# Optimization experiments

Measured on AMD Instinct MI355X. Metric: run time of the kernel, lower is better.

Reference implementation:

```python
import jax, jax.numpy as jnp
import numpy as np

D_MODEL = 1024
N_HEADS = 16
D_K = D_MODEL // N_HEADS


def _xavier(key, shape):
    fan_in, fan_out = shape[1], shape[0]
    a = np.sqrt(6.0 / (fan_in + fan_out))
    return jax.random.uniform(key, shape, jnp.float32, -a, a)


def setup_inputs() -> dict:
    key = jax.random.key(0)
    kx, kq, kk, kv, ko = jax.random.split(key, 5)
    x = jax.random.normal(kx, (2, 2048, D_MODEL), jnp.float32)
    # nn.Linear weights are [out, in]; y = x @ W.T
    Wq = _xavier(kq, (D_MODEL, D_MODEL))
    Wk = _xavier(kk, (D_MODEL, D_MODEL))
    Wv = _xavier(kv, (D_MODEL, D_MODEL))
    Wo = _xavier(ko, (D_MODEL, D_MODEL))
    bo = jnp.zeros((D_MODEL,), jnp.float32)
    return {"x": x, "Wq": Wq, "Wk": Wk, "Wv": Wv, "Wo": Wo, "bo": bo}


def reference(x, Wq, Wk, Wv, Wo, bo):
    B, S, D = x.shape
    def split_heads(t):
        # [B,S,D] -> [B,H,S,d_k]
        return t.reshape(B, S, N_HEADS, D_K).transpose(0, 2, 1, 3)
    Q = split_heads(x @ Wq.T)
    K = split_heads(x @ Wk.T)
    V = split_heads(x @ Wv.T)
    scale = 1.0 / jnp.sqrt(jnp.asarray(D_K, x.dtype))
    scores = jnp.einsum('bhqd,bhkd->bhqk', Q, K) * scale  # [B,H,S,S]
    attn = jax.nn.softmax(scores, axis=-1)
    out = jnp.einsum('bhqk,bhkd->bhqd', attn, V)  # [B,H,S,d_k]
    out = out.transpose(0, 2, 1, 3).reshape(B, S, D)  # merge heads
    return out @ Wo.T + bo
```

## Files before the change

### kernel.cpp

```cpp
#include <hip/hip_runtime.h>


typedef __attribute__((ext_vector_type(8))) short bf16x8;
typedef __attribute__((ext_vector_type(4))) short bf16x4;
typedef __attribute__((ext_vector_type(4))) float f32x4;
typedef __attribute__((ext_vector_type(2))) unsigned int u32x2;
typedef __attribute__((ext_vector_type(4))) unsigned int u32x4;

#define GK 1024
#define SEQ 2048
#define NHEAD 16
#define DKD 64
#define PADW 72

#define MFMA32(a, b, c) __builtin_amdgcn_mfma_f32_16x16x32_bf16((a), (b), (c), 0, 0, 0)

#if __has_builtin(__builtin_amdgcn_exp2f)
#define EXP2(x) __builtin_amdgcn_exp2f(x)
#else
#define EXP2(x) exp2f(x)
#endif

#define QSCALE 0.18033688011f

static __device__ __forceinline__ unsigned short f2bf(float f) {
    unsigned int u = __float_as_uint(f);
    u += 0x7fffu + ((u >> 16) & 1u);
    return (unsigned short)(u >> 16);
}

static __device__ __forceinline__ unsigned int pack_bf2(float a, float b) {
    unsigned int ua = __float_as_uint(a) + 0x8000u;
    unsigned int ub = __float_as_uint(b) + 0x8000u;
    return __builtin_amdgcn_perm(ub, ua, 0x07060302u);
}

__global__ __launch_bounds__(256) void cast_all(const float* __restrict__ x,
                                                const float* __restrict__ wq,
                                                const float* __restrict__ wk,
                                                const float* __restrict__ wv,
                                                const float* __restrict__ wo,
                                                unsigned short* __restrict__ Xb,
                                                unsigned short* __restrict__ Wqkv,
                                                unsigned short* __restrict__ Wob) {
    const int bid = blockIdx.x;
    const float* src; unsigned short* dst; int off;
    if (bid < 4096)      { src = x;  dst = Xb;             off = bid; }
    else if (bid < 5120) { src = wq; dst = Wqkv;           off = bid - 4096; }
    else if (bid < 6144) { src = wk; dst = Wqkv + 1048576; off = bid - 5120; }
    else if (bid < 7168) { src = wv; dst = Wqkv + 2097152; off = bid - 6144; }
    else                 { src = wo; dst = Wob;            off = bid - 7168; }
    const int i = off * 1024 + threadIdx.x * 4;
    float4 v = *(const float4*)(src + i);
    u32x2 p; p.x = pack_bf2(v.x, v.y); p.y = pack_bf2(v.z, v.w);
    *(u32x2*)(dst + i) = p;
}

template <int MODE, int BN>
__global__ __launch_bounds__(256) void gemm_bt(const unsigned short* __restrict__ A,
                                               const unsigned short* __restrict__ Bw,
                                               unsigned short* __restrict__ outb,
                                               float* __restrict__ outf,
                                               const float* __restrict__ bias) {
    constexpr int NJ = BN / 32;
    constexpr int LOOP_BYTES = 128 * 64 * 2 + BN * 64 * 2;
    constexpr int EPI_BYTES  = 4 * 64 * PADW * 2;
    constexpr int SMEM_BYTES = (MODE == 0)
        ? (LOOP_BYTES > EPI_BYTES ? LOOP_BYTES : EPI_BYTES)
        : LOOP_BYTES;
    __shared__ __align__(16) unsigned char SMEM[SMEM_BYTES];
    unsigned short* As = (unsigned short*)SMEM;
    unsigned short* Bs = As + 128 * 64;

    const int t    = threadIdx.x;
    const int lane = t & 63;
    const int w    = t >> 6;
    const int wm   = (w >> 1) * 64;
    const int wn   = (w & 1) * (BN / 2);
    const int bm0  = blockIdx.x * 128;
    const int bn0  = blockIdx.y * BN;
    const int lm   = lane & 15;
    const int lq   = lane >> 4;
    const int swzb = lm & 7;

    const unsigned short* Ab = A + (size_t)bm0 * GK;
    const unsigned short* Bb = Bw + (size_t)bn0 * GK;

    f32x4 acc[4][NJ];
    const f32x4 Z4 = {0.f, 0.f, 0.f, 0.f};
#pragma unroll
    for (int i = 0; i < 4; i++)
#pragma unroll
        for (int j = 0; j < NJ; j++) acc[i][j] = Z4;

    const int q_uni = (t & ~63);

    for (int k0 = 0; k0 < GK; k0 += 64) {
        __syncthreads();
#pragma unroll
        for (int i = 0; i < 4; ++i) {
            int q  = i * 256 + t;
            int r  = q >> 3;
            int gc = (q & 7) ^ (r & 7);
            int q0 = i * 256 + q_uni;
            __builtin_amdgcn_global_load_lds(
                (const __attribute__((address_space(1))) void*)(Ab + (size_t)r * GK + k0 + gc * 8),
                (__attribute__((address_space(3))) void*)(As + (size_t)q0 * 8),
                16, 0, 0);
        }
#pragma unroll
        for (int i = 0; i < BN / 32; ++i) {
            int q  = i * 256 + t;
            int r  = q >> 3;
            int gc = (q & 7) ^ (r & 7);
            int q0 = i * 256 + q_uni;
            __builtin_amdgcn_global_load_lds(
                (const __attribute__((address_space(1))) void*)(Bb + (size_t)r * GK + k0 + gc * 8),
                (__attribute__((address_space(3))) void*)(Bs + (size_t)q0 * 8),
                16, 0, 0);
        }
        __syncthreads();

#pragma unroll
        for (int kk = 0; kk < 2; ++kk) {
            const int swz = ((kk * 4 + lq) ^ swzb) * 8;
            bf16x8 af[4], bf[NJ];
#pragma unroll
            for (int i = 0; i < 4; i++)
                af[i] = *(const bf16x8*)(As + (wm + i * 16 + lm) * 64 + swz);
#pragma unroll
            for (int j = 0; j < NJ; j++)
                bf[j] = *(const bf16x8*)(Bs + (wn + j * 16 + lm) * 64 + swz);
#pragma unroll
            for (int i = 0; i < 4; i++)
#pragma unroll
                for (int j = 0; j < NJ; j++)
                    acc[i][j] = MFMA32(af[i], bf[j], acc[i][j]);
        }
    }

    if (MODE == 0) {
        __syncthreads();
        unsigned short* E  = (unsigned short*)SMEM;
        unsigned short* Ew = E + w * (64 * PADW);
        const int nbase = bn0 + wn;
        const int which = nbase >> 10;
        const int hh    = (nbase & 1023) >> 6;
        if (which != 2) {
            const float sc = (which == 0) ? QSCALE : 1.0f;
#pragma unroll
            for (int i = 0; i < 4; i++)
#pragma unroll
                for (int j = 0; j < 4; j++)
#pragma unroll
                    for (int r = 0; r < 4; r++)
                        Ew[(i * 16 + lq * 4 + r) * PADW + j * 16 + lm] =
                            f2bf(acc[i][j][r] * sc);
            unsigned short* dst = outb + (size_t)which * 4194304;
#pragma unroll
            for (int rep = 0; rep < 8; ++rep) {
                const int mm = rep * 8 + (lane >> 3);
                const int d0 = (lane & 7) * 8;
                uint4 v = *(const uint4*)(Ew + mm * PADW + d0);
                const int m_g = bm0 + wm + mm;
                const int b = m_g >> 11, s = m_g & 2047;
                *(uint4*)(dst + (((size_t)(b * NHEAD + hh)) * SEQ + s) * DKD + d0) = v;
            }
        } else {
#pragma unroll
            for (int i = 0; i < 4; i++)
#pragma unroll
                for (int j = 0; j < 4; j++) {
                    u32x2 pk;
                    pk.x = pack_bf2(acc[i][j][0], acc[i][j][1]);
                    pk.y = pack_bf2(acc[i][j][2], acc[i][j][3]);
                    *(u32x2*)(Ew + (j * 16 + lm) * PADW + i * 16 + lq * 4) = pk;
                }
            unsigned short* dst = outb + (size_t)2 * 4194304;
#pragma unroll
            for (int rep = 0; rep < 8; ++rep) {
                const int nn = rep * 8 + (lane >> 3);
                const int mc = (lane & 7) * 8;
                uint4 v = *(const uint4*)(Ew + nn * PADW + mc);
                const int m_g = bm0 + wm + mc;
                const int b = m_g >> 11, s0 = m_g & 2047;
                *(uint4*)(dst + (((size_t)(b * NHEAD + hh)) * DKD + nn) * SEQ + s0) = v;
            }
        }
    } else {
#pragma unroll
        for (int i = 0; i < 4; i++) {
            const int mbase = bm0 + wm + i * 16 + lq * 4;
#pragma unroll
            for (int j = 0; j < NJ; j++) {
                const int n = bn0 + wn + j * 16 + lm;
#pragma unroll
                for (int r = 0; r < 4; r++)
                    outf[(size_t)(mbase + r) * 1024 + n] = acc[i][j][r] + bias[n];
            }
        }
    }
}

__global__ __launch_bounds__(256, 4) void attn_kernel(const unsigned short* __restrict__ Qg,
                                                      const unsigned short* __restrict__ Kg,
                                                      const unsigned short* __restrict__ Vtg,
                                                      unsigned short* __restrict__ Og) {
    __shared__ __align__(16) unsigned short KV[2][2][64 * PADW];

    const int id  = blockIdx.x;
    const int xcd = id & 7;
    const int j8  = id >> 3;
    const int bh  = xcd * 4 + (j8 & 3);
    const int qb  = j8 >> 2;
    const unsigned short* Qp  = Qg  + ((size_t)bh * SEQ + qb * 64) * DKD;
    const unsigned short* Kp  = Kg  + (size_t)bh * SEQ * DKD;
    const unsigned short* Vtp = Vtg + (size_t)bh * DKD * SEQ;

    const int t    = threadIdx.x;
    const int lane = t & 63;
    const int w    = t >> 6;
    const int qg   = w >> 1;
    const int kg   = w & 1;
    const int lm   = lane & 15;
    const int kq   = lane >> 4;

    const f32x4 Z4 = {0.f, 0.f, 0.f, 0.f};

    bf16x8 aq[2][2];
#pragma unroll
    for (int c = 0; c < 2; ++c)
#pragma unroll
        for (int kk = 0; kk < 2; ++kk)
            aq[c][kk] = *(const bf16x8*)(Qp + (size_t)(qg * 32 + c * 16 + lm) * DKD + kk * 32 + kq * 8);

    f32x4 o[2][4];
    float ls[2];
#pragma unroll
    for (int c = 0; c < 2; ++c) {
        ls[c] = 0.f;
#pragma unroll
        for (int dj = 0; dj < 4; ++dj) o[c][dj] = Z4;
    }

    const int sr = t >> 2, sc = (t & 3) * 16;
    uint4 kreg0, kreg1, vreg0, vreg1;
    {
        const unsigned short* kp = Kp + (size_t)sr * DKD + sc;
        const unsigned short* vp = Vtp + (size_t)sr * SEQ + sc;
        uint4 a0 = *(const uint4*)(kp), a1 = *(const uint4*)(kp + 8);
        uint4 b0 = *(const uint4*)(vp), b1 = *(const uint4*)(vp + 8);
        uint4* dk = (uint4*)(&KV[0][0][sr * PADW + sc]); dk[0] = a0; dk[1] = a1;
        uint4* dv = (uint4*)(&KV[0][1][sr * PADW + sc]); dv[0] = b0; dv[1] = b1;
    }
    {
        const unsigned short* kp = Kp + (size_t)(64 + sr) * DKD + sc;
        kreg0 = *(const uint4*)(kp); kreg1 = *(const uint4*)(kp + 8);
        const unsigned short* vp = Vtp + (size_t)sr * SEQ + 64 + sc;
        vreg0 = *(const uint4*)(vp); vreg1 = *(const uint4*)(vp + 8);
    }

    for (int kt = 0; kt < 32; ++kt) {
        asm volatile("s_waitcnt lgkmcnt(0)\n\ts_barrier" ::: "memory");
        const unsigned short* Kc = &KV[kt & 1][0][0];
        const unsigned short* Vc = &KV[kt & 1][1][0];

        bf16x8 ak[2][2];
#pragma unroll
        for (int kc = 0; kc < 2; ++kc)
#pragma unroll
            for (int kk = 0; kk < 2; ++kk)
                ak[kc][kk] = *(const bf16x8*)(Kc + (kg * 32 + kc * 16 + lm) * PADW + kk * 32 + kq * 8);

        if (kt + 1 < 32) {
            uint4* dk = (uint4*)(&KV[(kt + 1) & 1][0][sr * PADW + sc]);
            dk[0] = kreg0; dk[1] = kreg1;
            uint4* dv = (uint4*)(&KV[(kt + 1) & 1][1][sr * PADW + sc]);
            dv[0] = vreg0; dv[1] = vreg1;
        }
        if (kt + 2 < 32) {
            const unsigned short* kp = Kp + (size_t)((kt + 2) * 64 + sr) * DKD + sc;
            kreg0 = *(const uint4*)(kp); kreg1 = *(const uint4*)(kp + 8);
            const unsigned short* vp = Vtp + (size_t)sr * SEQ + (kt + 2) * 64 + sc;
            vreg0 = *(const uint4*)(vp); vreg1 = *(const uint4*)(vp + 8);
        }

        f32x4 s[2][2];
        __builtin_amdgcn_s_setprio(1);
#pragma unroll
        for (int kc = 0; kc < 2; ++kc)
#pragma unroll
            for (int c = 0; c < 2; ++c) {
                s[kc][c] = MFMA32(ak[kc][0], aq[c][0], Z4);
                s[kc][c] = MFMA32(ak[kc][1], aq[c][1], s[kc][c]);
            }
        __builtin_amdgcn_s_setprio(0);

        bf16x8 bv[4];
#pragma unroll
        for (int dj = 0; dj < 4; ++dj) {
            const unsigned short* vr = Vc + (dj * 16 + lm) * PADW + kg * 32;
            u32x2 lo = __builtin_bit_cast(u32x2, *(const bf16x4*)(vr + kq * 4));
            u32x2 hi = __builtin_bit_cast(u32x2, *(const bf16x4*)(vr + 16 + kq * 4));
            u32x4 uu; uu.x = lo.x; uu.y = lo.y; uu.z = hi.x; uu.w = hi.y;
            bv[dj] = __builtin_bit_cast(bf16x8, uu);
        }

#pragma unroll
        for (int c = 0; c < 2; ++c) {
#pragma unroll
            for (int kc = 0; kc < 2; ++kc)
#pragma unroll
                for (int r = 0; r < 4; ++r) s[kc][c][r] = EXP2(s[kc][c][r]);
            ls[c] += ((s[0][c][0] + s[0][c][1]) + (s[0][c][2] + s[0][c][3]))
                   + ((s[1][c][0] + s[1][c][1]) + (s[1][c][2] + s[1][c][3]));
        }

        bf16x8 pa[2];
#pragma unroll
        for (int c = 0; c < 2; ++c) {
            u32x4 uu;
            uu.x = pack_bf2(s[0][c][0], s[0][c][1]);
            uu.y = pack_bf2(s[0][c][2], s[0][c][3]);
            uu.z = pack_bf2(s[1][c][0], s[1][c][1]);
            uu.w = pack_bf2(s[1][c][2], s[1][c][3]);
            pa[c] = __builtin_bit_cast(bf16x8, uu);
        }

        __builtin_amdgcn_s_setprio(1);
#pragma unroll
        for (int dj = 0; dj < 4; ++dj)
#pragma unroll
            for (int c = 0; c < 2; ++c)
                o[c][dj] = MFMA32(pa[c], bv[dj], o[c][dj]);
        __builtin_amdgcn_s_setprio(0);
    }

    __syncthreads();
    float* Lf = (float*)(&KV[0][0][0]);

#pragma unroll
    for (int c = 0; c < 2; ++c) {
        float v = ls[c];
        v += __shfl_xor(v, 16);
        v += __shfl_xor(v, 32);
        if (kq == 0) Lf[w * 32 + c * 16 + lm] = v;
    }
    __syncthreads();

    const int rq = t >> 2;
    const int dq = (t & 3) * 8;
    const int qgr = rq >> 5, qlr = rq & 31;
    float li = Lf[qgr * 64 + qlr] + Lf[qgr * 64 + 32 + qlr];
#if __has_builtin(__builtin_amdgcn_rcpf)
    li = __builtin_amdgcn_rcpf(li);
#else
    li = 1.0f / li;
#endif
    __syncthreads();

    const int b = bh >> 4, h = bh & 15;
#pragma unroll
    for (int p = 0; p < 2; ++p) {
#pragma unroll
        for (int c = 0; c < 2; ++c)
#pragma unroll
            for (int djh = 0; djh < 2; ++djh) {
                const int dj = 2 * p + djh;
#pragma unroll
                for (int r = 0; r < 4; ++r)
                    Lf[(w * 32 + c * 16 + kq * 4 + r) * 36 + djh * 16 + lm] = o[c][dj][r];
            }
        __syncthreads();
        f32x4 a0 = *(const f32x4*)(Lf + (qgr * 64 + qlr) * 36 + dq)
                 + *(const f32x4*)(Lf + (qgr * 64 + 32 + qlr) * 36 + dq);
        f32x4 a1 = *(const f32x4*)(Lf + (qgr * 64 + qlr) * 36 + dq + 4)
                 + *(const f32x4*)(Lf + (qgr * 64 + 32 + qlr) * 36 + dq + 4);
        uint4 outv;
        outv.x = pack_bf2(a0[0] * li, a0[1] * li);
        outv.y = pack_bf2(a0[2] * li, a0[3] * li);
        outv.z = pack_bf2(a1[0] * li, a1[1] * li);
        outv.w = pack_bf2(a1[2] * li, a1[3] * li);
        *(uint4*)(Og + (((size_t)(b * SEQ + qb * 64 + rq)) * NHEAD + h) * DKD + p * 32 + dq) = outv;
        __syncthreads();
    }
}

extern "C" void kernel_launch(void* const* d_in, const int* in_sizes, int n_in,
                              void* d_out, int out_size, void* d_ws, size_t ws_size,
                              hipStream_t stream) {
    const float* x  = (const float*)d_in[0];
    const float* Wq = (const float*)d_in[1];
    const float* Wk = (const float*)d_in[2];
    const float* Wv = (const float*)d_in[3];
    const float* Wo = (const float*)d_in[4];
    const float* bo = (const float*)d_in[5];
    float* out = (float*)d_out;

    unsigned short* ws = (unsigned short*)d_ws;
    unsigned short* Xb   = ws;
    unsigned short* Wqkv = ws + 4194304;
    unsigned short* Wob  = ws + 7340032;
    unsigned short* QKV  = ws + 8388608;
    unsigned short* Ob   = ws + 20971520;

    cast_all<<<8192, 256, 0, stream>>>(x, Wq, Wk, Wv, Wo, Xb, Wqkv, Wob);
    gemm_bt<0, 128><<<dim3(32, 24), 256, 0, stream>>>(Xb, Wqkv, QKV, nullptr, nullptr);
    attn_kernel<<<1024, 256, 0, stream>>>(QKV, QKV + 4194304, QKV + 8388608, Ob);
    gemm_bt<1, 64><<<dim3(32, 16), 256, 0, stream>>>(Ob, Wob, nullptr, out, bo);
}
```

Before: 187.5 us.

## Process 128 query rows per attention block to reuse K/V tiles

Each attention block now handles two 64-row query halves against the same K/V tiles staged in shared memory. This halves the grid to 512 blocks and halves the total K/V global and LDS staging traffic per query row. The cost is doubled accumulator and Q register state, with the launch-bounds occupancy hint lowered from 4 to 2. Fewer blocks are also available to fill the GPU.

```diff
diff --git a/kernel.cpp b/kernel.cpp
--- a/kernel.cpp
+++ b/kernel.cpp
@@ -202,7 +202,7 @@
     }
 }
 
-__global__ __launch_bounds__(256, 4) void attn_kernel(const unsigned short* __restrict__ Qg,
+__global__ __launch_bounds__(256, 2) void attn_kernel(const unsigned short* __restrict__ Qg,
                                                       const unsigned short* __restrict__ Kg,
                                                       const unsigned short* __restrict__ Vtg,
                                                       unsigned short* __restrict__ Og) {
@@ -213,7 +213,7 @@
     const int j8  = id >> 3;
     const int bh  = xcd * 4 + (j8 & 3);
     const int qb  = j8 >> 2;
-    const unsigned short* Qp  = Qg  + ((size_t)bh * SEQ + qb * 64) * DKD;
+    const unsigned short* Qp  = Qg  + ((size_t)bh * SEQ + qb * 128) * DKD;
     const unsigned short* Kp  = Kg  + (size_t)bh * SEQ * DKD;
     const unsigned short* Vtp = Vtg + (size_t)bh * DKD * SEQ;
 
@@ -227,21 +227,25 @@
 
     const f32x4 Z4 = {0.f, 0.f, 0.f, 0.f};
 
-    bf16x8 aq[2][2];
-#pragma unroll
-    for (int c = 0; c < 2; ++c)
-#pragma unroll
-        for (int kk = 0; kk < 2; ++kk)
-            aq[c][kk] = *(const bf16x8*)(Qp + (size_t)(qg * 32 + c * 16 + lm) * DKD + kk * 32 + kq * 8);
-
-    f32x4 o[2][4];
-    float ls[2];
-#pragma unroll
-    for (int c = 0; c < 2; ++c) {
-        ls[c] = 0.f;
-#pragma unroll
-        for (int dj = 0; dj < 4; ++dj) o[c][dj] = Z4;
-    }
+    bf16x8 aq[2][2][2];
+#pragma unroll
+    for (int h2 = 0; h2 < 2; ++h2)
+#pragma unroll
+        for (int c = 0; c < 2; ++c)
+#pragma unroll
+            for (int kk = 0; kk < 2; ++kk)
+                aq[h2][c][kk] = *(const bf16x8*)(Qp + (size_t)(h2 * 64 + qg * 32 + c * 16 + lm) * DKD + kk * 32 + kq * 8);
+
+    f32x4 o[2][2][4];
+    float ls[2][2];
+#pragma unroll
+    for (int h2 = 0; h2 < 2; ++h2)
+#pragma unroll
+        for (int c = 0; c < 2; ++c) {
+            ls[h2][c] = 0.f;
+#pragma unroll
+            for (int dj = 0; dj < 4; ++dj) o[h2][c][dj] = Z4;
+        }
 
     const int sr = t >> 2, sc = (t & 3) * 16;
     uint4 kreg0, kreg1, vreg0, vreg1;
@@ -285,17 +289,6 @@
             vreg0 = *(const uint4*)(vp); vreg1 = *(const uint4*)(vp + 8);
         }
 
-        f32x4 s[2][2];
-        __builtin_amdgcn_s_setprio(1);
-#pragma unroll
-        for (int kc = 0; kc < 2; ++kc)
-#pragma unroll
-            for (int c = 0; c < 2; ++c) {
-                s[kc][c] = MFMA32(ak[kc][0], aq[c][0], Z4);
-                s[kc][c] = MFMA32(ak[kc][1], aq[c][1], s[kc][c]);
-            }
-        __builtin_amdgcn_s_setprio(0);
-
         bf16x8 bv[4];
 #pragma unroll
         for (int dj = 0; dj < 4; ++dj) {
@@ -307,81 +300,106 @@
         }
 
 #pragma unroll
-        for (int c = 0; c < 2; ++c) {
+        for (int h2 = 0; h2 < 2; ++h2) {
+            f32x4 s[2][2];
+            __builtin_amdgcn_s_setprio(1);
 #pragma unroll
             for (int kc = 0; kc < 2; ++kc)
 #pragma unroll
-                for (int r = 0; r < 4; ++r) s[kc][c][r] = EXP2(s[kc][c][r]);
-            ls[c] += ((s[0][c][0] + s[0][c][1]) + (s[0][c][2] + s[0][c][3]))
-                   + ((s[1][c][0] + s[1][c][1]) + (s[1][c][2] + s[1][c][3]));
-        }
-
-        bf16x8 pa[2];
-#pragma unroll
-        for (int c = 0; c < 2; ++c) {
-            u32x4 uu;
-            uu.x = pack_bf2(s[0][c][0], s[0][c][1]);
-            uu.y = pack_bf2(s[0][c][2], s[0][c][3]);
-            uu.z = pack_bf2(s[1][c][0], s[1][c][1]);
-            uu.w = pack_bf2(s[1][c][2], s[1][c][3]);
-            pa[c] = __builtin_bit_cast(bf16x8, uu);
-        }
-
-        __builtin_amdgcn_s_setprio(1);
-#pragma unroll
-        for (int dj = 0; dj < 4; ++dj)
-#pragma unroll
-            for (int c = 0; c < 2; ++c)
-                o[c][dj] = MFMA32(pa[c], bv[dj], o[c][dj]);
-        __builtin_amdgcn_s_setprio(0);
+                for (int c = 0; c < 2; ++c) {
+                    s[kc][c] = MFMA32(ak[kc][0], aq[h2][c][0], Z4);
+                    s[kc][c] = MFMA32(ak[kc][1], aq[h2][c][1], s[kc][c]);
+                }
+            __builtin_amdgcn_s_setprio(0);
+
+#pragma unroll
+            for (int c = 0; c < 2; ++c) {
+#pragma unroll
+                for (int kc = 0; kc < 2; ++kc)
+#pragma unroll
+                    for (int r = 0; r < 4; ++r) s[kc][c][r] = EXP2(s[kc][c][r]);
+                ls[h2][c] += ((s[0][c][0] + s[0][c][1]) + (s[0][c][2] + s[0][c][3]))
+                           + ((s[1][c][0] + s[1][c][1]) + (s[1][c][2] + s[1][c][3]));
+            }
+
+            bf16x8 pa[2];
+#pragma unroll
+            for (int c = 0; c < 2; ++c) {
+                u32x4 uu;
+                uu.x = pack_bf2(s[0][c][0], s[0][c][1]);
+                uu.y = pack_bf2(s[0][c][2], s[0][c][3]);
+                uu.z = pack_bf2(s[1][c][0], s[1][c][1]);
+                uu.w = pack_bf2(s[1][c][2], s[1][c][3]);
+                pa[c] = __builtin_bit_cast(bf16x8, uu);
+            }
+
+            __builtin_amdgcn_s_setprio(1);
+#pragma unroll
+            for (int dj = 0; dj < 4; ++dj)
+#pragma unroll
+                for (int c = 0; c < 2; ++c)
+                    o[h2][c][dj] = MFMA32(pa[c], bv[dj], o[h2][c][dj]);
+            __builtin_amdgcn_s_setprio(0);
+        }
     }
 
     __syncthreads();
     float* Lf = (float*)(&KV[0][0][0]);
 
 #pragma unroll
-    for (int c = 0; c < 2; ++c) {
-        float v = ls[c];
-        v += __shfl_xor(v, 16);
-        v += __shfl_xor(v, 32);
-        if (kq == 0) Lf[w * 32 + c * 16 + lm] = v;
-    }
+    for (int h2 = 0; h2 < 2; ++h2)
+#pragma unroll
+        for (int c = 0; c < 2; ++c) {
+            float v = ls[h2][c];
+            v += __shfl_xor(v, 16);
+            v += __shfl_xor(v, 32);
+            if (kq == 0) Lf[(h2 * 4 + w) * 32 + c * 16 + lm] = v;
+        }
     __syncthreads();
 
     const int rq = t >> 2;
     const int dq = (t & 3) * 8;
     const int qgr = rq >> 5, qlr = rq & 31;
-    float li = Lf[qgr * 64 + qlr] + Lf[qgr * 64 + 32 + qlr];
+    float li[2];
+#pragma unroll
+    for (int h2 = 0; h2 < 2; ++h2) {
+        float l = Lf[(h2 * 4 + qgr * 2) * 32 + qlr] + Lf[(h2 * 4 + qgr * 2 + 1) * 32 + qlr];
 #if __has_builtin(__builtin_amdgcn_rcpf)
-    li = __builtin_amdgcn_rcpf(li);
+        li[h2] = __builtin_amdgcn_rcpf(l);
 #else
-    li = 1.0f / li;
+        li[h2] = 1.0f / l;
 #endif
+    }
     __syncthreads();
 
     const int b = bh >> 4, h = bh & 15;
 #pragma unroll
     for (int p = 0; p < 2; ++p) {
 #pragma unroll
-        for (int c = 0; c < 2; ++c)
-#pragma unroll
-            for (int djh = 0; djh < 2; ++djh) {
-                const int dj = 2 * p + djh;
-#pragma unroll
-                for (int r = 0; r < 4; ++r)
-                    Lf[(w * 32 + c * 16 + kq * 4 + r) * 36 + djh * 16 + lm] = o[c][dj][r];
-            }
+        for (int h2 = 0; h2 < 2; ++h2)
+#pragma unroll
+            for (int c = 0; c < 2; ++c)
+#pragma unroll
+                for (int djh = 0; djh < 2; ++djh) {
+                    const int dj = 2 * p + djh;
+#pragma unroll
+                    for (int r = 0; r < 4; ++r)
+                        Lf[((h2 * 4 + w) * 32 + c * 16 + kq * 4 + r) * 36 + djh * 16 + lm] = o[h2][c][dj][r];
+                }
         __syncthreads();
-        f32x4 a0 = *(const f32x4*)(Lf + (qgr * 64 + qlr) * 36 + dq)
-                 + *(const f32x4*)(Lf + (qgr * 64 + 32 + qlr) * 36 + dq);
-        f32x4 a1 = *(const f32x4*)(Lf + (qgr * 64 + qlr) * 36 + dq + 4)
-                 + *(const f32x4*)(Lf + (qgr * 64 + 32 + qlr) * 36 + dq + 4);
-        uint4 outv;
-        outv.x = pack_bf2(a0[0] * li, a0[1] * li);
-        outv.y = pack_bf2(a0[2] * li, a0[3] * li);
-        outv.z = pack_bf2(a1[0] * li, a1[1] * li);
-        outv.w = pack_bf2(a1[2] * li, a1[3] * li);
-        *(uint4*)(Og + (((size_t)(b * SEQ + qb * 64 + rq)) * NHEAD + h) * DKD + p * 32 + dq) = outv;
+#pragma unroll
+        for (int h2 = 0; h2 < 2; ++h2) {
+            const int rowA = ((h2 * 4 + qgr * 2) * 32 + qlr) * 36;
+            const int rowB = ((h2 * 4 + qgr * 2 + 1) * 32 + qlr) * 36;
+            f32x4 a0 = *(const f32x4*)(Lf + rowA + dq) + *(const f32x4*)(Lf + rowB + dq);
+            f32x4 a1 = *(const f32x4*)(Lf + rowA + dq + 4) + *(const f32x4*)(Lf + rowB + dq + 4);
+            uint4 outv;
+            outv.x = pack_bf2(a0[0] * li[h2], a0[1] * li[h2]);
+            outv.y = pack_bf2(a0[2] * li[h2], a0[3] * li[h2]);
+            outv.z = pack_bf2(a1[0] * li[h2], a1[1] * li[h2]);
+            outv.w = pack_bf2(a1[2] * li[h2], a1[3] * li[h2]);
+            *(uint4*)(Og + (((size_t)(b * SEQ + qb * 128 + h2 * 64 + rq)) * NHEAD + h) * DKD + p * 32 + dq) = outv;
+        }
         __syncthreads();
     }
 }
@@ -406,6 +424,6 @@
 
     cast_all<<<8192, 256, 0, stream>>>(x, Wq, Wk, Wv, Wo, Xb, Wqkv, Wob);
     gemm_bt<0, 128><<<dim3(32, 24), 256, 0, stream>>>(Xb, Wqkv, QKV, nullptr, nullptr);
-    attn_kernel<<<1024, 256, 0, stream>>>(QKV, QKV + 4194304, QKV + 8388608, Ob);
+    attn_kernel<<<512, 256, 0, stream>>>(QKV, QKV + 4194304, QKV + 8388608, Ob);
     gemm_bt<1, 64><<<dim3(32, 16), 256, 0, stream>>>(Ob, Wob, nullptr, out, bo);
 }
```

Result: faster. 181.5 us (-3.2%).
